# Kernel optimization log

Measured on AMD Instinct MI355X. Metric: run time of the kernel, lower is better.

## Reference

```python
import jax, jax.numpy as jnp
import numpy as np

NEG_BIG = -9e15
ALPHA = 0.2  # leakyrelu negative slope

N, F_IN, F_OUT = 8192, 512, 64


def setup_inputs() -> dict:
    key = jax.random.key(0)
    k1, k2, k3, k4 = jax.random.split(key, 4)
    input = jax.random.normal(k1, (N, F_IN), dtype=jnp.float32)
    adj = jax.random.randint(k2, (N, N), 0, 2, dtype=jnp.int32)
    W = jax.random.normal(k3, (F_IN, F_OUT), dtype=jnp.float32) * 0.05
    a = jax.random.normal(k4, (2 * F_OUT, 1), dtype=jnp.float32) * 0.1
    return {"input": input, "adj": adj, "W": W, "a": a}


def reference(input, adj, W, a):
    # h: [N, F_out]
    h = input @ W
    # The original builds a_input[i,j] = concat(h_i, h_j) and dots with a.
    # Decompose: e_ij = leakyrelu(h_i @ a_src + h_j @ a_dst) -- identical math,
    # avoids the N*N*2F intermediate.
    a_src = a[:F_OUT, 0]  # [F_out]
    a_dst = a[F_OUT:, 0]  # [F_out]
    s_src = h @ a_src     # [N]
    s_dst = h @ a_dst     # [N]
    e = jax.nn.leaky_relu(s_src[:, None] + s_dst[None, :], negative_slope=ALPHA)  # [N, N]
    masked = jnp.where(adj > 0, e, jnp.float32(NEG_BIG))
    attention = jax.nn.softmax(masked, axis=1)  # dropout omitted (eval mode)
    h_prime = attention @ h  # [N, F_out]
    return jax.nn.elu(h_prime)  # concat=True
```

## Files before the change

### kernel.cpp

```cpp
#include <hip/hip_runtime.h>
#include <hip/hip_bf16.h>

namespace {
constexpr int kN    = 8192;
constexpr int kFin  = 512;
constexpr int kFout = 64;
constexpr float kAlpha = 0.2f;

using bf16x8 = __attribute__((ext_vector_type(8))) short;
using f32x4  = __attribute__((ext_vector_type(4))) float;

__device__ __forceinline__ unsigned short f2bf(float x) {
  return __builtin_bit_cast(unsigned short, __float2bfloat16(x));
}
}

__global__ __launch_bounds__(256) void k_linear(
    const float* __restrict__ X, const float* __restrict__ W, const float* __restrict__ A,
    unsigned short* __restrict__ hT, float* __restrict__ s_src, float* __restrict__ s_dst)
{
  const int t = threadIdx.x;
  const int wv = t >> 6, lane = t & 63;
  const int i0 = blockIdx.x * 16;
  const int r0 = i0 + wv * 4;
  float acc0 = 0.f, acc1 = 0.f, acc2 = 0.f, acc3 = 0.f;
  const float* x0 = X + (size_t)r0 * kFin;
  for (int k = 0; k < kFin; k += 4) {
    const float4 xa = *(const float4*)(x0 + k);
    const float4 xb = *(const float4*)(x0 + kFin + k);
    const float4 xc = *(const float4*)(x0 + 2 * kFin + k);
    const float4 xd = *(const float4*)(x0 + 3 * kFin + k);
#pragma unroll
    for (int j = 0; j < 4; ++j) {
      const float wk = W[(k + j) * kFout + lane];
      acc0 = fmaf(((const float*)&xa)[j], wk, acc0);
      acc1 = fmaf(((const float*)&xb)[j], wk, acc1);
      acc2 = fmaf(((const float*)&xc)[j], wk, acc2);
      acc3 = fmaf(((const float*)&xd)[j], wk, acc3);
    }
  }
  const float asrc = A[lane], adst = A[kFout + lane];
  float accs[4] = {acc0, acc1, acc2, acc3};
#pragma unroll
  for (int r = 0; r < 4; ++r) {
    float vs = accs[r] * asrc;
    float vd = accs[r] * adst;
#pragma unroll
    for (int off = 32; off > 0; off >>= 1) {
      vs += __shfl_xor(vs, off, 64);
      vd += __shfl_xor(vd, off, 64);
    }
    if (lane == 0) { s_src[r0 + r] = vs; s_dst[r0 + r] = vd; }
  }
  __shared__ unsigned short h_sm[16][64];
#pragma unroll
  for (int r = 0; r < 4; ++r) h_sm[wv * 4 + r][lane] = f2bf(accs[r]);
  __syncthreads();
  const int f = t >> 2, io = (t & 3) * 4;
  const unsigned int u0 = (unsigned int)h_sm[io + 0][f] | ((unsigned int)h_sm[io + 1][f] << 16);
  const unsigned int u1 = (unsigned int)h_sm[io + 2][f] | ((unsigned int)h_sm[io + 3][f] << 16);
  *(uint2*)(hT + (size_t)f * kN + i0 + io) = make_uint2(u0, u1);
}

__global__ __launch_bounds__(1024) void k_smax(const float* __restrict__ s_dst,
                                               float* __restrict__ Sout)
{
  __shared__ float red[16];
  float m = -3.4e38f;
  for (int i = threadIdx.x; i < kN; i += 1024) m = fmaxf(m, s_dst[i]);
#pragma unroll
  for (int off = 32; off > 0; off >>= 1) m = fmaxf(m, __shfl_xor(m, off, 64));
  if ((threadIdx.x & 63) == 0) red[threadIdx.x >> 6] = m;
  __syncthreads();
  if (threadIdx.x == 0) {
    float s = red[0];
#pragma unroll
    for (int i = 1; i < 16; ++i) s = fmaxf(s, red[i]);
    *Sout = s;
  }
}

__global__ __launch_bounds__(256) void k_attn(
    const int* __restrict__ adj, const unsigned short* __restrict__ hTg,
    const float* __restrict__ s_src, const float* __restrict__ s_dst,
    const float* __restrict__ Sp, float* __restrict__ out)
{
  const int t = threadIdx.x;
  const int wv = t >> 6, lane = t & 63;
  const int i0 = blockIdx.x * 16;
  const int pr = t >> 4, jb = t & 15;
  const int hf = t >> 2, hs = t & 3;

  __shared__ unsigned short Plds[16][136];
  __shared__ unsigned short Hlds[64][136];
  __shared__ float l_sm[16];

  const float S = *Sp;
  const float ssrc = s_src[i0 + pr];
  float mr = ssrc + S;
  mr = mr > 0.f ? mr : kAlpha * mr;

  float l_acc = 0.f;
  f32x4 acc = {0.f, 0.f, 0.f, 0.f};

  const size_t adj_off = (size_t)(i0 + pr) * kN + (size_t)jb * 8;
  const size_t hT_off  = (size_t)hf * kN + (size_t)hs * 32;

  int4 A0, A1; float4 d0, d1; uint4 hv0, hv1, hv2, hv3;
  auto load_chunk = [&](int c) {
    const int j0 = c * 128;
    const int4* ap = (const int4*)(adj + adj_off + j0);
    A0 = ap[0]; A1 = ap[1];
    const float* dp = s_dst + j0 + jb * 8;
    d0 = *(const float4*)dp;
    d1 = *(const float4*)(dp + 4);
    const uint4* hp = (const uint4*)(hTg + hT_off + (size_t)j0);
    hv0 = hp[0]; hv1 = hp[1]; hv2 = hp[2]; hv3 = hp[3];
  };
  load_chunk(0);

  const int mrow = lane & 15, quad = lane >> 4;
  for (int c = 0; c < kN / 128; ++c) {
    float pv[8];
    {
      const int* aa = (const int*)&A0;
      const float* dd = (const float*)&d0;
#pragma unroll
      for (int j = 0; j < 4; ++j) {
        float x = ssrc + dd[j];
        float e = x > 0.f ? x : kAlpha * x;
        pv[j] = aa[j] > 0 ? __expf(e - mr) : 0.f;
      }
      aa = (const int*)&A1; dd = (const float*)&d1;
#pragma unroll
      for (int j = 0; j < 4; ++j) {
        float x = ssrc + dd[j];
        float e = x > 0.f ? x : kAlpha * x;
        pv[4 + j] = aa[j] > 0 ? __expf(e - mr) : 0.f;
      }
    }
    bf16x8 ps;
#pragma unroll
    for (int j = 0; j < 8; ++j) {
      l_acc += pv[j];
      ps[j] = (short)f2bf(pv[j]);
    }
    *(bf16x8*)&Plds[pr][jb * 8] = ps;
    *(uint4*)&Hlds[hf][hs * 32 + 0]  = hv0;
    *(uint4*)&Hlds[hf][hs * 32 + 8]  = hv1;
    *(uint4*)&Hlds[hf][hs * 32 + 16] = hv2;
    *(uint4*)&Hlds[hf][hs * 32 + 24] = hv3;
    __syncthreads();

    if (c + 1 < kN / 128) load_chunk(c + 1);

#pragma unroll
    for (int ks = 0; ks < 4; ++ks) {
      bf16x8 av = *(const bf16x8*)&Plds[mrow][ks * 32 + quad * 8];
      bf16x8 bv = *(const bf16x8*)&Hlds[wv * 16 + mrow][ks * 32 + quad * 8];
      acc = __builtin_amdgcn_mfma_f32_16x16x32_bf16(av, bv, acc, 0, 0, 0);
    }
    __syncthreads();
  }

  float lv = l_acc;
  lv += __shfl_xor(lv, 8, 64);
  lv += __shfl_xor(lv, 4, 64);
  lv += __shfl_xor(lv, 2, 64);
  lv += __shfl_xor(lv, 1, 64);
  if (jb == 0) l_sm[pr] = lv;
  __syncthreads();

#pragma unroll
  for (int reg = 0; reg < 4; ++reg) {
    const int r = quad * 4 + reg;
    float v = acc[reg] / l_sm[r];
    v = v > 0.f ? v : __expf(v) - 1.f;
    out[(size_t)(i0 + r) * kFout + wv * 16 + mrow] = v;
  }
}

extern "C" void kernel_launch(void* const* d_in, const int* in_sizes, int n_in,
                              void* d_out, int out_size, void* d_ws, size_t ws_size,
                              hipStream_t stream) {
  const float* X   = (const float*)d_in[0];
  const int*   adj = (const int*)d_in[1];
  const float* W   = (const float*)d_in[2];
  const float* A   = (const float*)d_in[3];
  float* out = (float*)d_out;

  unsigned short* hT = (unsigned short*)d_ws;
  float* s_src = (float*)((char*)d_ws + (size_t)kFout * kN * 2);
  float* s_dst = s_src + kN;
  float* Sp    = s_dst + kN;

  k_linear<<<kN / 16, 256, 0, stream>>>(X, W, A, hT, s_src, s_dst);
  k_smax<<<1, 1024, 0, stream>>>(s_dst, Sp);
  k_attn<<<kN / 16, 256, 0, stream>>>(adj, hT, s_src, s_dst, Sp, out);
}
```

Baseline: 423.0 us.

## Split attention over column chunks and read h in MFMA-ready layout from global

The attention kernel is split along the neighbour dimension into four partial blocks per row tile, and a new combine kernel sums the partial accumulators and row sums, then applies the normalisation and ELU. The linear kernel now writes h in a fragment-ordered layout so the MFMA B operand loads straight from global memory, which removes the H staging in LDS. The P tile is double-buffered so one barrier per chunk can be dropped. The linear kernel also reads a pre-transposed W with vector loads, produced by a new small kernel. This adds launches and partial-sum traffic in exchange for more parallelism and less LDS synchronisation in the main loop, which is dominated by reading the adjacency matrix.

```diff
diff --git a/kernel.cpp b/kernel.cpp
--- a/kernel.cpp
+++ b/kernel.cpp
@@ -6,6 +6,9 @@
 constexpr int kFin  = 512;
 constexpr int kFout = 64;
 constexpr float kAlpha = 0.2f;
+constexpr int kJSplit = 4;
+constexpr int kJLen   = kN / kJSplit;
+constexpr int kChunks = kJLen / 128;
 
 using bf16x8 = __attribute__((ext_vector_type(8))) short;
 using f32x4  = __attribute__((ext_vector_type(4))) float;
@@ -13,36 +16,45 @@
 __device__ __forceinline__ unsigned short f2bf(float x) {
   return __builtin_bit_cast(unsigned short, __float2bfloat16(x));
 }
+__device__ __forceinline__ float lrelu(float x) {
+  return fmaxf(x, kAlpha * x);
+}
+}
+
+__global__ __launch_bounds__(256) void k_wt(const float* __restrict__ W,
+                                            float* __restrict__ WT) {
+  const int gid = blockIdx.x * 256 + threadIdx.x;
+  const int k = gid >> 6, f = gid & 63;
+  WT[(size_t)f * kFin + k] = W[gid];
 }
 
 __global__ __launch_bounds__(256) void k_linear(
-    const float* __restrict__ X, const float* __restrict__ W, const float* __restrict__ A,
-    unsigned short* __restrict__ hT, float* __restrict__ s_src, float* __restrict__ s_dst)
+    const float* __restrict__ X, const float* __restrict__ WT, const float* __restrict__ A,
+    unsigned short* __restrict__ hTf, float* __restrict__ s_src, float* __restrict__ s_dst)
 {
   const int t = threadIdx.x;
-  const int wv = t >> 6, lane = t & 63;
-  const int i0 = blockIdx.x * 16;
-  const int r0 = i0 + wv * 4;
-  float acc0 = 0.f, acc1 = 0.f, acc2 = 0.f, acc3 = 0.f;
+  const int rh = t >> 6, f = t & 63;
+  const int i0 = blockIdx.x * 8;
+  const int r0 = i0 + rh * 2;
+
   const float* x0 = X + (size_t)r0 * kFin;
+  const float* w0 = WT + (size_t)f * kFin;
+  float a0 = 0.f, a1 = 0.f;
   for (int k = 0; k < kFin; k += 4) {
+    const float4 wv = *(const float4*)(w0 + k);
     const float4 xa = *(const float4*)(x0 + k);
     const float4 xb = *(const float4*)(x0 + kFin + k);
-    const float4 xc = *(const float4*)(x0 + 2 * kFin + k);
-    const float4 xd = *(const float4*)(x0 + 3 * kFin + k);
 #pragma unroll
     for (int j = 0; j < 4; ++j) {
-      const float wk = W[(k + j) * kFout + lane];
-      acc0 = fmaf(((const float*)&xa)[j], wk, acc0);
-      acc1 = fmaf(((const float*)&xb)[j], wk, acc1);
-      acc2 = fmaf(((const float*)&xc)[j], wk, acc2);
-      acc3 = fmaf(((const float*)&xd)[j], wk, acc3);
-    }
-  }
-  const float asrc = A[lane], adst = A[kFout + lane];
-  float accs[4] = {acc0, acc1, acc2, acc3};
-#pragma unroll
-  for (int r = 0; r < 4; ++r) {
+      a0 = fmaf(((const float*)&xa)[j], ((const float*)&wv)[j], a0);
+      a1 = fmaf(((const float*)&xb)[j], ((const float*)&wv)[j], a1);
+    }
+  }
+
+  const float asrc = A[f], adst = A[kFout + f];
+  float accs[2] = {a0, a1};
+#pragma unroll
+  for (int r = 0; r < 2; ++r) {
     float vs = accs[r] * asrc;
     float vd = accs[r] * adst;
 #pragma unroll
@@ -50,16 +62,22 @@
       vs += __shfl_xor(vs, off, 64);
       vd += __shfl_xor(vd, off, 64);
     }
-    if (lane == 0) { s_src[r0 + r] = vs; s_dst[r0 + r] = vd; }
-  }
-  __shared__ unsigned short h_sm[16][64];
-#pragma unroll
-  for (int r = 0; r < 4; ++r) h_sm[wv * 4 + r][lane] = f2bf(accs[r]);
+    if (f == 0) { s_src[r0 + r] = vs; s_dst[r0 + r] = vd; }
+  }
+
+  __shared__ unsigned short h_sm[8][64];
+  h_sm[rh * 2 + 0][f] = f2bf(a0);
+  h_sm[rh * 2 + 1][f] = f2bf(a1);
   __syncthreads();
-  const int f = t >> 2, io = (t & 3) * 4;
-  const unsigned int u0 = (unsigned int)h_sm[io + 0][f] | ((unsigned int)h_sm[io + 1][f] << 16);
-  const unsigned int u1 = (unsigned int)h_sm[io + 2][f] | ((unsigned int)h_sm[io + 3][f] << 16);
-  *(uint2*)(hT + (size_t)f * kN + i0 + io) = make_uint2(u0, u1);
+  if (t < 64) {
+    const int w = t >> 4, fl = t & 15;
+    const int jblk = i0 >> 5, q = (i0 >> 3) & 3;
+    const int lane = q * 16 + fl;
+    bf16x8 v;
+#pragma unroll
+    for (int e = 0; e < 8; ++e) v[e] = (short)h_sm[e][w * 16 + fl];
+    *(bf16x8*)(hTf + (((size_t)jblk * 4 + w) * 64 + lane) * 8) = v;
+  }
 }
 
 __global__ __launch_bounds__(1024) void k_smax(const float* __restrict__ s_dst,
@@ -81,61 +99,55 @@
 }
 
 __global__ __launch_bounds__(256) void k_attn(
-    const int* __restrict__ adj, const unsigned short* __restrict__ hTg,
+    const int* __restrict__ adj, const unsigned short* __restrict__ hTf,
     const float* __restrict__ s_src, const float* __restrict__ s_dst,
-    const float* __restrict__ Sp, float* __restrict__ out)
+    const float* __restrict__ Sp, float* __restrict__ accp, float* __restrict__ lp)
 {
   const int t = threadIdx.x;
   const int wv = t >> 6, lane = t & 63;
-  const int i0 = blockIdx.x * 16;
+  const int b = blockIdx.x;
+  const int i0 = (b >> 2) * 16;
+  const int jbase = (b & 3) * kJLen;
   const int pr = t >> 4, jb = t & 15;
-  const int hf = t >> 2, hs = t & 3;
-
-  __shared__ unsigned short Plds[16][136];
-  __shared__ unsigned short Hlds[64][136];
-  __shared__ float l_sm[16];
+
+  __shared__ unsigned short Plds[2][16][136];
 
   const float S = *Sp;
   const float ssrc = s_src[i0 + pr];
-  float mr = ssrc + S;
-  mr = mr > 0.f ? mr : kAlpha * mr;
+  const float mr = lrelu(ssrc + S);
 
   float l_acc = 0.f;
   f32x4 acc = {0.f, 0.f, 0.f, 0.f};
 
-  const size_t adj_off = (size_t)(i0 + pr) * kN + (size_t)jb * 8;
-  const size_t hT_off  = (size_t)hf * kN + (size_t)hs * 32;
-
-  int4 A0, A1; float4 d0, d1; uint4 hv0, hv1, hv2, hv3;
+  const size_t adj_off = (size_t)(i0 + pr) * kN + jbase + (size_t)jb * 8;
+  int4 A0, A1; float4 d0, d1;
   auto load_chunk = [&](int c) {
-    const int j0 = c * 128;
-    const int4* ap = (const int4*)(adj + adj_off + j0);
+    const int4* ap = (const int4*)(adj + adj_off + (size_t)c * 128);
     A0 = ap[0]; A1 = ap[1];
-    const float* dp = s_dst + j0 + jb * 8;
-    d0 = *(const float4*)dp;
-    d1 = *(const float4*)(dp + 4);
-    const uint4* hp = (const uint4*)(hTg + hT_off + (size_t)j0);
-    hv0 = hp[0]; hv1 = hp[1]; hv2 = hp[2]; hv3 = hp[3];
+    const float* dp = s_dst + jbase + c * 128 + jb * 8;
+    d0 = ((const float4*)dp)[0];
+    d1 = ((const float4*)dp)[1];
   };
   load_chunk(0);
 
   const int mrow = lane & 15, quad = lane >> 4;
-  for (int c = 0; c < kN / 128; ++c) {
+  const unsigned short* hptr =
+      hTf + (((size_t)(jbase >> 5) * 4 + wv) * 64 + lane) * 8;
+
+  for (int c = 0; c < kChunks; ++c) {
     float pv[8];
     {
       const int* aa = (const int*)&A0;
       const float* dd = (const float*)&d0;
 #pragma unroll
       for (int j = 0; j < 4; ++j) {
-        float x = ssrc + dd[j];
-        float e = x > 0.f ? x : kAlpha * x;
+        const float e = lrelu(ssrc + dd[j]);
         pv[j] = aa[j] > 0 ? __expf(e - mr) : 0.f;
       }
       aa = (const int*)&A1; dd = (const float*)&d1;
 #pragma unroll
       for (int j = 0; j < 4; ++j) {
-        float x = ssrc + dd[j];
-        float e = x > 0.f ? x : kAlpha * x;
+        const float e = lrelu(ssrc + dd[j]);
         pv[4 + j] = aa[j] > 0 ? __expf(e - mr) : 0.f;
       }
     }
@@ -145,22 +157,15 @@
       l_acc += pv[j];
       ps[j] = (short)f2bf(pv[j]);
     }
-    *(bf16x8*)&Plds[pr][jb * 8] = ps;
-    *(uint4*)&Hlds[hf][hs * 32 + 0]  = hv0;
-    *(uint4*)&Hlds[hf][hs * 32 + 8]  = hv1;
-    *(uint4*)&Hlds[hf][hs * 32 + 16] = hv2;
-    *(uint4*)&Hlds[hf][hs * 32 + 24] = hv3;
+    *(bf16x8*)&Plds[c & 1][pr][jb * 8] = ps;
+    if (c + 1 < kChunks) load_chunk(c + 1);
     __syncthreads();
-
-    if (c + 1 < kN / 128) load_chunk(c + 1);
-
 #pragma unroll
     for (int ks = 0; ks < 4; ++ks) {
-      bf16x8 av = *(const bf16x8*)&Plds[mrow][ks * 32 + quad * 8];
-      bf16x8 bv = *(const bf16x8*)&Hlds[wv * 16 + mrow][ks * 32 + quad * 8];
+      const bf16x8 av = *(const bf16x8*)&Plds[c & 1][mrow][ks * 32 + quad * 8];
+      const bf16x8 bv = *(const bf16x8*)(hptr + ((size_t)c * 4 + ks) * 2048);
       acc = __builtin_amdgcn_mfma_f32_16x16x32_bf16(av, bv, acc, 0, 0, 0);
     }
-    __syncthreads();
   }
 
   float lv = l_acc;
@@ -168,16 +173,32 @@
   lv += __shfl_xor(lv, 4, 64);
   lv += __shfl_xor(lv, 2, 64);
   lv += __shfl_xor(lv, 1, 64);
-  if (jb == 0) l_sm[pr] = lv;
-  __syncthreads();
-
+  if (jb == 0) lp[(size_t)b * 16 + pr] = lv;
+
+  float* ab = accp + (size_t)b * 16 * 64;
 #pragma unroll
   for (int reg = 0; reg < 4; ++reg) {
-    const int r = quad * 4 + reg;
-    float v = acc[reg] / l_sm[r];
-    v = v > 0.f ? v : __expf(v) - 1.f;
-    out[(size_t)(i0 + r) * kFout + wv * 16 + mrow] = v;
-  }
+    ab[(quad * 4 + reg) * 64 + wv * 16 + mrow] = acc[reg];
+  }
+}
+
+__global__ __launch_bounds__(256) void k_comb(const float* __restrict__ accp,
+                                              const float* __restrict__ lp,
+                                              float* __restrict__ out)
+{
+  const int gid = blockIdx.x * 256 + threadIdx.x;
+  const int i = gid >> 6, f = gid & 63;
+  const int ib = i >> 4, il = i & 15;
+  const int b0 = ib * kJSplit;
+  float a = 0.f, l = 0.f;
+#pragma unroll
+  for (int q = 0; q < kJSplit; ++q) {
+    a += accp[((size_t)(b0 + q) * 16 + il) * 64 + f];
+    l += lp[(size_t)(b0 + q) * 16 + il];
+  }
+  float v = a / l;
+  v = v > 0.f ? v : __expf(v) - 1.f;
+  out[gid] = v;
 }
 
 extern "C" void kernel_launch(void* const* d_in, const int* in_sizes, int n_in,
@@ -189,12 +210,18 @@
   const float* A   = (const float*)d_in[3];
   float* out = (float*)d_out;
 
-  unsigned short* hT = (unsigned short*)d_ws;
-  float* s_src = (float*)((char*)d_ws + (size_t)kFout * kN * 2);
-  float* s_dst = s_src + kN;
-  float* Sp    = s_dst + kN;
-
-  k_linear<<<kN / 16, 256, 0, stream>>>(X, W, A, hT, s_src, s_dst);
-  k_smax<<<1, 1024, 0, stream>>>(s_dst, Sp);
-  k_attn<<<kN / 16, 256, 0, stream>>>(adj, hT, s_src, s_dst, Sp, out);
-}
+  char* ws = (char*)d_ws;
+  unsigned short* hTf = (unsigned short*)ws;              ws += (size_t)kN * kFout * 2;
+  float* WT    = (float*)ws;                              ws += (size_t)kFout * kFin * 4;
+  float* s_src = (float*)ws;                              ws += kN * 4;
+  float* s_dst = (float*)ws;                              ws += kN * 4;
+  float* Sp    = (float*)ws;                              ws += 256;
+  float* accp  = (float*)ws;                              ws += (size_t)(kN / 16) * kJSplit * 16 * 64 * 4;
+  float* lp    = (float*)ws;
+
+  k_wt    <<<kFin * kFout / 256, 256, 0, stream>>>(W, WT);
+  k_linear<<<kN / 8, 256, 0, stream>>>(X, WT, A, hTf, s_src, s_dst);
+  k_smax  <<<1, 1024, 0, stream>>>(s_dst, Sp);
+  k_attn  <<<(kN / 16) * kJSplit, 256, 0, stream>>>(adj, hTf, s_src, s_dst, Sp, accp, lp);
+  k_comb  <<<kN * kFout / 256, 256, 0, stream>>>(accp, lp, out);
+}
```

Result: slower. 458.0 us (+8.3%).
